# Kernel tuning notes

Hardware: AMD Instinct MI355X
Metric: run time of the kernel (lower is better)

The kernel has to match this reference:

```python
import jax, jax.numpy as jnp
import numpy as np

B, S, E = 2, 2048, 1024
H, D = 16, 64  # NUM_ATTENTION_HEADS, NUM_FEATURES
LN_EPS = 1e-5


def setup_inputs() -> dict:
    key = jax.random.key(0)
    ks = jax.random.split(key, 10)
    scale = 1.0 / np.sqrt(E)
    return {
        "x": jax.random.normal(ks[0], (B, S, E), dtype=jnp.float32),
        "ln_g": jnp.ones((E,), dtype=jnp.float32),
        "ln_b": jnp.zeros((E,), dtype=jnp.float32),
        "wq": jax.random.normal(ks[1], (E, H * D), dtype=jnp.float32) * scale,
        "bq": jnp.zeros((H * D,), dtype=jnp.float32),
        "wk": jax.random.normal(ks[2], (E, H * D), dtype=jnp.float32) * scale,
        "bk": jnp.zeros((H * D,), dtype=jnp.float32),
        "wv": jax.random.normal(ks[3], (E, H * D), dtype=jnp.float32) * scale,
        "bv": jnp.zeros((H * D,), dtype=jnp.float32),
        "wo": jax.random.normal(ks[4], (H * D, E), dtype=jnp.float32) * scale,
        "bo": jnp.zeros((E,), dtype=jnp.float32),
    }


def reference(x, ln_g, ln_b, wq, bq, wk, bk, wv, bv, wo, bo):
    x_residual = x
    # LayerNorm over last dim
    mean = jnp.mean(x, axis=-1, keepdims=True)
    var = jnp.mean(jnp.square(x - mean), axis=-1, keepdims=True)
    xn = (x - mean) * jax.lax.rsqrt(var + LN_EPS) * ln_g + ln_b

    q = (xn @ wq + bq).reshape(B, S, H, D)
    k = (xn @ wk + bk).reshape(B, S, H, D)
    v = (xn @ wv + bv).reshape(B, S, H, D)

    # scores: [B, S_q, S_k, H]
    score = jnp.einsum('bihd,bjhd->bijh', q, k) / np.sqrt(D).astype(np.float32)
    # causal mask: position i may not attend to j > i
    causal = jnp.tril(jnp.ones((S, S), dtype=bool))  # True = keep
    score = jnp.where(causal[None, :, :, None], score, -jnp.inf)
    probs = jax.nn.softmax(score, axis=2)

    out = jnp.einsum('bijh,bjhd->bihd', probs, v).reshape(B, S, H * D)
    out = out @ wo + bo
    return out + x_residual
```

## Files before the change

kernel.cpp:

```cpp
#include <hip/hip_runtime.h>
#include <math.h>
#include <stdint.h>

typedef short short8 __attribute__((ext_vector_type(8)));
typedef short s16x4 __attribute__((ext_vector_type(4)));
typedef float f32x4 __attribute__((ext_vector_type(4)));

constexpr int BB = 2, SS = 2048, EE = 1024, HH = 16, DD = 64, HD = 1024;
constexpr int NROW = BB * SS;
constexpr size_t WELEM = (size_t)1024 * 1024;
constexpr float LN_EPS = 1e-5f;

__device__ const int ENT_QT[40] = {0,1,2,3, 4,4, 5,5, 6,6, 7,7,
                                   8,8,8, 9,9,9, 10,10,10, 11,11,11,
                                   12,12,12,12, 13,13,13,13, 14,14,14,14, 15,15,15,15};
__device__ const int ENT_C0[40] = {0,0,0,0, 0,1, 0,1, 0,1, 0,1,
                                   0,1,2, 0,1,2, 0,1,2, 0,1,2,
                                   0,1,2,3, 0,1,2,3, 0,1,2,3, 0,1,2,3};
__device__ const int EBASE[16]  = {0,1,2,3,4,6,8,10,12,15,18,21,24,28,32,36};
constexpr int NENT = 40;

#if defined(__has_builtin)
#if __has_builtin(__builtin_amdgcn_exp2f)
#define EXP2F(x) __builtin_amdgcn_exp2f(x)
#endif
#endif
#ifndef EXP2F
#define EXP2F(x) exp2f(x)
#endif

__device__ inline short f2bf(float f) {
    union { float f; uint32_t u; } v; v.f = f;
    uint32_t r = (v.u + 0x7fffu + ((v.u >> 16) & 1u)) >> 16;
    return (short)(uint16_t)r;
}

__device__ inline float bf2f(short s) {
    return __uint_as_float(((uint32_t)(uint16_t)s) << 16);
}

__device__ inline uint32_t pk2bf(float f0, float f1) {
    uint32_t u0 = __float_as_uint(f0) + 0x8000u;
    uint32_t u1 = __float_as_uint(f1) + 0x8000u;
    return __builtin_amdgcn_perm(u1, u0, 0x07060302u);
}

__device__ inline uint32_t pk2bf_t(float f0, float f1) {
    return __builtin_amdgcn_perm(__float_as_uint(f1), __float_as_uint(f0), 0x07060302u);
}

__device__ inline s16x4 pack_bf16x4(f32x4 v) {
    union { uint32_t u[2]; s16x4 s; } r;
    r.u[0] = pk2bf(v[0], v[1]);
    r.u[1] = pk2bf(v[2], v[3]);
    return r.s;
}

#define GLOBAL_TO_LDS16(g, l) \
    __builtin_amdgcn_global_load_lds( \
        (const __attribute__((address_space(1))) void*)(g), \
        (__attribute__((address_space(3))) void*)(l), 16, 0, 0)

__global__ void prep_kernel(const float* __restrict__ x,
                            const float* __restrict__ g,
                            const float* __restrict__ b,
                            short* __restrict__ xn,
                            const float* __restrict__ w0, const float* __restrict__ w1,
                            const float* __restrict__ w2, const float* __restrict__ w3,
                            short* __restrict__ wdst) {
    const int bx = blockIdx.x;
    const int t = threadIdx.x;
    if (bx < NROW) {
        const int row = bx;
        const float* xr = x + (size_t)row * EE;
        short* onr = xn + (size_t)row * EE;
        float4 v = ((const float4*)xr)[t];
        float s  = v.x + v.y + v.z + v.w;
        float ss = v.x * v.x + v.y * v.y + v.z * v.z + v.w * v.w;
        #pragma unroll
        for (int o = 32; o > 0; o >>= 1) {
            s  += __shfl_down(s, o);
            ss += __shfl_down(ss, o);
        }
        __shared__ float sm[4], sm2[4];
        const int wid = t >> 6, lane = t & 63;
        if (lane == 0) { sm[wid] = s; sm2[wid] = ss; }
        __syncthreads();
        float ts  = sm[0] + sm[1] + sm[2] + sm[3];
        float tss = sm2[0] + sm2[1] + sm2[2] + sm2[3];
        float mean = ts * (1.0f / EE);
        float var  = tss * (1.0f / EE) - mean * mean;
        float inv  = rsqrtf(var + LN_EPS);
        float4 gv = ((const float4*)g)[t];
        float4 bv = ((const float4*)b)[t];
        s16x4 st;
        st.x = f2bf((v.x - mean) * inv * gv.x + bv.x);
        st.y = f2bf((v.y - mean) * inv * gv.y + bv.y);
        st.z = f2bf((v.z - mean) * inv * gv.z + bv.z);
        st.w = f2bf((v.w - mean) * inv * gv.w + bv.w);
        ((s16x4*)onr)[t] = st;
    } else {
        const int widx = bx - NROW;
        const int z = widx >> 10;
        const int rem = widx & 1023;
        const int k0 = (rem >> 5) * 32, p0 = (rem & 31) * 32;
        const float* src = (z == 0) ? w0 : (z == 1) ? w1 : (z == 2) ? w2 : w3;
        short* d = wdst + (size_t)z * WELEM;
        __shared__ float tile[32][33];
        const int tx = t & 31, ty = t >> 5;
        #pragma unroll
        for (int r = ty; r < 32; r += 8)
            tile[r][tx] = src[(size_t)(k0 + r) * 1024 + p0 + tx];
        __syncthreads();
        #pragma unroll
        for (int r = ty; r < 32; r += 8)
            d[(size_t)(p0 + r) * 1024 + k0 + tx] = f2bf(tile[tx][r]);
    }
}

template <bool F32OUT>
__global__ __launch_bounds__(256) void mfma_gemm(
    const short* __restrict__ A,
    const short* __restrict__ BtBase,
    const float* __restrict__ b0, const float* __restrict__ b1,
    const float* __restrict__ b2,
    short* __restrict__ outB, short* __restrict__ outV,
    const float* __restrict__ resid, float* __restrict__ outF) {
    constexpr int K = 1024, N = 1024;
    const int t = threadIdx.x, lane = t & 63, w = t >> 6;
    const int quad = lane >> 4, l16 = lane & 15;
    const int wm = w >> 1, wn = w & 1;
    const int row0 = blockIdx.y * 128, col0 = blockIdx.x * 128;
    const int z = blockIdx.z;
    const short* Bt = BtBase + (size_t)z * WELEM;
    const float* bias = (z == 0) ? b0 : (z == 1) ? b1 : b2;

    __shared__ short As[128 * 32];
    __shared__ short Bs[128 * 32];

    f32x4 acc[4][4];
    #pragma unroll
    for (int i = 0; i < 4; i++)
        #pragma unroll
        for (int j = 0; j < 4; j++) acc[i][j] = (f32x4){0.f, 0.f, 0.f, 0.f};

    const int srow = t >> 2, schunk = t & 3;
    const short* agp = A  + (size_t)(row0 + srow) * K + schunk * 8;
    const short* bgp = Bt + (size_t)(col0 + srow) * K + schunk * 8;

    for (int k0 = 0; k0 < K; k0 += 32) {
        GLOBAL_TO_LDS16(agp + k0,                    As + t * 8);
        GLOBAL_TO_LDS16(agp + (size_t)64 * K + k0,   As + 2048 + t * 8);
        GLOBAL_TO_LDS16(bgp + k0,                    Bs + t * 8);
        GLOBAL_TO_LDS16(bgp + (size_t)64 * K + k0,   Bs + 2048 + t * 8);
        __syncthreads();
        short8 af[4], bf[4];
        #pragma unroll
        for (int mt = 0; mt < 4; mt++)
            af[mt] = *(const short8*)&As[(wm * 64 + mt * 16 + l16) * 32 + quad * 8];
        #pragma unroll
        for (int nt = 0; nt < 4; nt++)
            bf[nt] = *(const short8*)&Bs[(wn * 64 + nt * 16 + l16) * 32 + quad * 8];
        #pragma unroll
        for (int mt = 0; mt < 4; mt++)
            #pragma unroll
            for (int nt = 0; nt < 4; nt++)
                acc[mt][nt] = __builtin_amdgcn_mfma_f32_16x16x32_bf16(
                    af[mt], bf[nt], acc[mt][nt], 0, 0, 0);
        __syncthreads();
    }

    #pragma unroll
    for (int mt = 0; mt < 4; mt++) {
        #pragma unroll
        for (int nt = 0; nt < 4; nt++) {
            const int rbase = row0 + wm * 64 + mt * 16 + quad * 4;
            const int col = col0 + wn * 64 + nt * 16 + l16;
            const float bcol = bias[col];
            if (F32OUT) {
                #pragma unroll
                for (int r = 0; r < 4; r++)
                    outF[(size_t)(rbase + r) * N + col] =
                        acc[mt][nt][r] + bcol +
                        resid[(size_t)(rbase + r) * N + col];
            } else if (z == 2) {
                union { uint32_t u[2]; s16x4 s; } pk;
                pk.u[0] = pk2bf(acc[mt][nt][0] + bcol, acc[mt][nt][1] + bcol);
                pk.u[1] = pk2bf(acc[mt][nt][2] + bcol, acc[mt][nt][3] + bcol);
                *(s16x4*)&outV[(size_t)col * NROW + rbase] = pk.s;
            } else {
                #pragma unroll
                for (int r = 0; r < 4; r++)
                    outB[(size_t)z * NROW * N + (size_t)(rbase + r) * N + col] =
                        f2bf(acc[mt][nt][r] + bcol);
            }
        }
    }
}

#define ATTN_ITER(JT, DIAG)                                                     \
    {                                                                           \
        const int jt_ = (JT);                                                   \
        if (jt_ + 1 < jt1) {                                                    \
            const size_t ko = (size_t)(jt_ + 1) * 64 * HD;                      \
            const int vo = (jt_ + 1) * 64;                                      \
            const int ob = (buf ^ 1) * 4096;                                    \
            GLOBAL_TO_LDS16(kb0 + ko, Kb + ob + t * 8);                         \
            GLOBAL_TO_LDS16(kb1 + ko, Kb + ob + (t + 256) * 8);                 \
            GLOBAL_TO_LDS16(vb0 + vo, Vb + ob + t * 8);                         \
            GLOBAL_TO_LDS16(vb1 + vo, Vb + ob + (t + 256) * 8);                 \
        }                                                                       \
        const short* Kc = Kb + buf * 4096;                                      \
        const short* Vc = Vb + buf * 4096;                                      \
        f32x4 s[4][2];                                                          \
        _Pragma("unroll")                                                       \
        for (int mj = 0; mj < 4; mj++)                                          \
            _Pragma("unroll")                                                   \
            for (int nt = 0; nt < 2; nt++) s[mj][nt] = (f32x4){0.f,0.f,0.f,0.f};\
        _Pragma("unroll")                                                       \
        for (int ks = 0; ks < 2; ks++) {                                        \
            const int cq = ((ks * 4 + quad) ^ sw) * 8;                          \
            short8 kf[4], qf[2];                                                \
            _Pragma("unroll")                                                   \
            for (int mj = 0; mj < 4; mj++)                                      \
                kf[mj] = *(const short8*)&Kc[(mj * 16 + l16) * 64 + cq];        \
            _Pragma("unroll")                                                   \
            for (int nt = 0; nt < 2; nt++)                                      \
                qf[nt] = *(const short8*)&Qs[(w * 32 + nt * 16 + l16) * 64 + cq];\
            _Pragma("unroll")                                                   \
            for (int mj = 0; mj < 4; mj++)                                      \
                _Pragma("unroll")                                               \
                for (int nt = 0; nt < 2; nt++)                                  \
                    s[mj][nt] = __builtin_amdgcn_mfma_f32_16x16x32_bf16(        \
                        kf[mj], qf[nt], s[mj][nt], 0, 0, 0);                    \
        }                                                                       \
        const int joff = (jt_ - 2 * qt) * 64;                                   \
        _Pragma("unroll")                                                       \
        for (int mj = 0; mj < 4; mj++) {                                        \
            _Pragma("unroll")                                                   \
            for (int nt = 0; nt < 2; nt++) {                                    \
                const int ir = irel + nt * 16;                                  \
                _Pragma("unroll")                                               \
                for (int r = 0; r < 4; r++) {                                   \
                    float p = EXP2F(s[mj][nt][r] * 0.18033688f);                \
                    if (DIAG) {                                                 \
                        const int jrel = joff + mj * 16 + quad * 4 + r;         \
                        if (jrel > ir) p = 0.f;                                 \
                    }                                                           \
                    s[mj][nt][r] = p;                                           \
                }                                                               \
            }                                                                   \
        }                                                                       \
        _Pragma("unroll")                                                       \
        for (int ks2 = 0; ks2 < 4; ks2++) {                                     \
            s16x4 pf[2];                                                        \
            _Pragma("unroll")                                                   \
            for (int nt = 0; nt < 2; nt++) {                                    \
                union { uint32_t u[2]; s16x4 s4; } r_;                          \
                r_.u[0] = pk2bf_t(s[ks2][nt][0], s[ks2][nt][1]);                \
                r_.u[1] = pk2bf_t(s[ks2][nt][2], s[ks2][nt][3]);                \
                pf[nt] = r_.s4;                                                 \
                Lacc[nt] = __builtin_amdgcn_mfma_f32_16x16x16bf16_1k(           \
                    onesf, pf[nt], Lacc[nt], 0, 0, 0);                          \
            }                                                                   \
            _Pragma("unroll")                                                   \
            for (int mtd = 0; mtd < 4; mtd++) {                                 \
                const int cv = (((ks2 * 2 + (quad >> 1)) ^ sw) * 8) + (quad & 1) * 4;\
                s16x4 vf = *(const s16x4*)&Vc[(mtd * 16 + l16) * 64 + cv];      \
                _Pragma("unroll")                                               \
                for (int nt = 0; nt < 2; nt++)                                  \
                    Ot[mtd][nt] = __builtin_amdgcn_mfma_f32_16x16x16bf16_1k(    \
                        vf, pf[nt], Ot[mtd][nt], 0, 0, 0);                      \
            }                                                                   \
        }                                                                       \
        __syncthreads();                                                        \
        buf ^= 1;                                                               \
    }

__global__ __launch_bounds__(256) void attn_split(
    const short* __restrict__ q, const short* __restrict__ kkk,
    const short* __restrict__ vtp,
    short* __restrict__ OpartB, float* __restrict__ lpart,
    short* __restrict__ attno) {
    const int e = NENT - 1 - (int)blockIdx.x;
    const int h = blockIdx.y, b = blockIdx.z;
    const int qt = ENT_QT[e], c0 = ENT_C0[e];
    const int t = threadIdx.x, lane = t & 63, w = t >> 6;
    const int quad = lane >> 4, l16 = lane & 15;
    const int sw = l16 & 7;
    const int i0 = qt * 128;

    __shared__ short Qs[128 * 64];
    __shared__ short Kb[2 * 64 * 64];
    __shared__ short Vb[2 * 64 * 64];

    const size_t qoff = ((size_t)(b * SS + i0)) * HD + h * DD;
    #pragma unroll
    for (int p = 0; p < 4; p++) {
        const int idx = t + p * 256;
        const int r = idx >> 3, cs = idx & 7;
        const int c = cs ^ (r & 7);
        GLOBAL_TO_LDS16(q + qoff + (size_t)r * HD + c * 8, Qs + idx * 8);
    }

    const int r0 = t >> 3,         cs0 = t & 7;
    const int r1 = (t + 256) >> 3, cs1 = (t + 256) & 7;
    const short* kb0 = kkk + ((size_t)b * SS) * HD + h * DD + (size_t)r0 * HD + (cs0 ^ (r0 & 7)) * 8;
    const short* kb1 = kkk + ((size_t)b * SS) * HD + h * DD + (size_t)r1 * HD + (cs1 ^ (r1 & 7)) * 8;
    const short* vb0 = vtp + ((size_t)(h * 64 + r0)) * NROW + b * SS + (cs0 ^ (r0 & 7)) * 8;
    const short* vb1 = vtp + ((size_t)(h * 64 + r1)) * NROW + b * SS + (cs1 ^ (r1 & 7)) * 8;

    f32x4 Ot[4][2];
    f32x4 Lacc[2];
    #pragma unroll
    for (int mtd = 0; mtd < 4; mtd++)
        #pragma unroll
        for (int nt = 0; nt < 2; nt++) Ot[mtd][nt] = (f32x4){0.f, 0.f, 0.f, 0.f};
    Lacc[0] = (f32x4){0.f, 0.f, 0.f, 0.f};
    Lacc[1] = (f32x4){0.f, 0.f, 0.f, 0.f};
    s16x4 onesf;
    onesf[0] = onesf[1] = onesf[2] = onesf[3] = (short)0x3F80;

    const int jt0 = c0 * 8;
    const int jt1 = min(jt0 + 8, 2 * qt + 2);
    const int irel = w * 32 + l16;

    {
        const size_t ko = (size_t)jt0 * 64 * HD;
        const int vo = jt0 * 64;
        GLOBAL_TO_LDS16(kb0 + ko, Kb + t * 8);
        GLOBAL_TO_LDS16(kb1 + ko, Kb + (t + 256) * 8);
        GLOBAL_TO_LDS16(vb0 + vo, Vb + t * 8);
        GLOBAL_TO_LDS16(vb1 + vo, Vb + (t + 256) * 8);
    }
    __syncthreads();

    int buf = 0;
    const int dmid   = min(jt1, 2 * qt);
    const int dstart = max(jt0, 2 * qt);
    for (int jt = jt0; jt < dmid; ++jt) ATTN_ITER(jt, false)
    for (int jt = dstart; jt < jt1; ++jt) ATTN_ITER(jt, true)

    if (qt < 4) {
        #pragma unroll
        for (int nt = 0; nt < 2; nt++) {
            const float inv = 1.0f / Lacc[nt][0];
            const int i_abs = i0 + w * 32 + nt * 16 + l16;
            const size_t ob = ((size_t)(b * SS + i_abs)) * HD + h * DD;
            #pragma unroll
            for (int mtd = 0; mtd < 4; mtd++) {
                f32x4 val = Ot[mtd][nt];
                union { uint32_t u[2]; s16x4 s4; } pk;
                pk.u[0] = pk2bf(val[0] * inv, val[1] * inv);
                pk.u[1] = pk2bf(val[2] * inv, val[3] * inv);
                *(s16x4*)&attno[ob + mtd * 16 + quad * 4] = pk.s4;
            }
        }
    } else {
        const int slot = (b * HH + h) * NENT + e;
        #pragma unroll
        for (int nt = 0; nt < 2; nt++) {
            const int i_rel = w * 32 + nt * 16 + l16;
            if (quad == 0) lpart[(size_t)slot * 128 + i_rel] = Lacc[nt][0];
            #pragma unroll
            for (int mtd = 0; mtd < 4; mtd++)
                *(s16x4*)&OpartB[(size_t)slot * 8192 + i_rel * 64 + mtd * 16 + quad * 4] =
                    pack_bf16x4(Ot[mtd][nt]);
        }
    }
}

__global__ __launch_bounds__(256) void attn_reduce(
    const short* __restrict__ OpartB, const float* __restrict__ lpart,
    short* __restrict__ attno) {
    const int qt = 4 + blockIdx.x, h = blockIdx.y, b = blockIdx.z;
    const int t = threadIdx.x;
    const int nch = (qt >> 2) + 1;
    const int slot0 = (b * HH + h) * NENT + EBASE[qt];
    const int i0 = qt * 128;
    #pragma unroll
    for (int it = 0; it < 8; it++) {
        const int g = t + it * 256;
        const int i = g >> 4, d4 = (g & 15) * 4;
        f32x4 acc = (f32x4){0.f, 0.f, 0.f, 0.f};
        float l = 0.f;
        for (int c = 0; c < nch; c++) {
            s16x4 pv = *(const s16x4*)&OpartB[(size_t)(slot0 + c) * 8192 + i * 64 + d4];
            acc[0] += bf2f(pv[0]);
            acc[1] += bf2f(pv[1]);
            acc[2] += bf2f(pv[2]);
            acc[3] += bf2f(pv[3]);
            l += lpart[(size_t)(slot0 + c) * 128 + i];
        }
        const float inv = 1.0f / l;
        union { uint32_t u[2]; s16x4 s; } pk;
        pk.u[0] = pk2bf(acc[0] * inv, acc[1] * inv);
        pk.u[1] = pk2bf(acc[2] * inv, acc[3] * inv);
        *(s16x4*)&attno[((size_t)(b * SS + i0 + i)) * HD + h * DD + d4] = pk.s;
    }
}

extern "C" void kernel_launch(void* const* d_in, const int* in_sizes, int n_in,
                              void* d_out, int out_size, void* d_ws, size_t ws_size,
                              hipStream_t stream) {
    const float* x    = (const float*)d_in[0];
    const float* ln_g = (const float*)d_in[1];
    const float* ln_b = (const float*)d_in[2];
    const float* wq   = (const float*)d_in[3];
    const float* bq   = (const float*)d_in[4];
    const float* wk   = (const float*)d_in[5];
    const float* bk   = (const float*)d_in[6];
    const float* wv   = (const float*)d_in[7];
    const float* bv   = (const float*)d_in[8];
    const float* wo   = (const float*)d_in[9];
    const float* bo   = (const float*)d_in[10];
    float* out = (float*)d_out;

    const size_t buf = (size_t)NROW * HD;
    short* xn    = (short*)d_ws;
    short* qb    = xn + buf;
    short* vt    = qb + 2 * buf;
    short* attno = vt + buf;
    short* wt    = attno + buf;
    short* OpB   = wt + 4 * WELEM;
    float* lpart = (float*)(OpB + (size_t)BB * HH * NENT * 8192);

    prep_kernel<<<2 * NROW, 256, 0, stream>>>(x, ln_g, ln_b, xn, wq, wk, wv, wo, wt);

    mfma_gemm<false><<<dim3(8, 32, 3), 256, 0, stream>>>(
        xn, wt, bq, bk, bv, qb, vt, nullptr, nullptr);

    attn_split<<<dim3(NENT, HH, BB), 256, 0, stream>>>(
        qb, qb + buf, vt, OpB, lpart, attno);
    attn_reduce<<<dim3(12, HH, BB), 256, 0, stream>>>(OpB, lpart, attno);

    mfma_gemm<true><<<dim3(8, 32, 1), 256, 0, stream>>>(
        attno, wt + 3 * WELEM, bo, bo, bo, nullptr, nullptr, x, out);
}
```

Before: 207.6 us.

## Fuse split-K attention reduction into attn_split via atomic counters; keep Q in registers

Removes the separate attn_reduce launch. Each split block writes its partial results, then bumps a per-(b,h,qt) atomic counter, and the last-arriving block performs the reduction and normalisation. The counters are zeroed in prep_kernel. Q fragments are now loaded straight into registers instead of being staged through LDS, and launch bounds request 4 blocks per SM. This saves a kernel launch and LDS traffic, at the cost of threadfence/atomic overhead and higher register pressure.

```diff
diff --git a/kernel.cpp b/kernel.cpp
--- a/kernel.cpp
+++ b/kernel.cpp
@@ -67,10 +67,14 @@
                             short* __restrict__ xn,
                             const float* __restrict__ w0, const float* __restrict__ w1,
                             const float* __restrict__ w2, const float* __restrict__ w3,
-                            short* __restrict__ wdst) {
+                            short* __restrict__ wdst, int* __restrict__ cnt) {
     const int bx = blockIdx.x;
     const int t = threadIdx.x;
     if (bx < NROW) {
+        if (bx == 0) {
+            cnt[t] = 0;
+            if (t < 128) cnt[256 + t] = 0;
+        }
         const int row = bx;
         const float* xr = x + (size_t)row * EE;
         short* onr = xn + (size_t)row * EE;
@@ -220,19 +224,16 @@
         _Pragma("unroll")                                                       \
         for (int ks = 0; ks < 2; ks++) {                                        \
             const int cq = ((ks * 4 + quad) ^ sw) * 8;                          \
-            short8 kf[4], qf[2];                                                \
+            short8 kf[4];                                                       \
             _Pragma("unroll")                                                   \
             for (int mj = 0; mj < 4; mj++)                                      \
                 kf[mj] = *(const short8*)&Kc[(mj * 16 + l16) * 64 + cq];        \
-            _Pragma("unroll")                                                   \
-            for (int nt = 0; nt < 2; nt++)                                      \
-                qf[nt] = *(const short8*)&Qs[(w * 32 + nt * 16 + l16) * 64 + cq];\
             _Pragma("unroll")                                                   \
             for (int mj = 0; mj < 4; mj++)                                      \
                 _Pragma("unroll")                                               \
                 for (int nt = 0; nt < 2; nt++)                                  \
                     s[mj][nt] = __builtin_amdgcn_mfma_f32_16x16x32_bf16(        \
-                        kf[mj], qf[nt], s[mj][nt], 0, 0, 0);                    \
+                        kf[mj], qreg[nt][ks], s[mj][nt], 0, 0, 0);              \
         }                                                                       \
         const int joff = (jt_ - 2 * qt) * 64;                                   \
         _Pragma("unroll")                                                       \
@@ -277,11 +278,11 @@
         buf ^= 1;                                                               \
     }
 
-__global__ __launch_bounds__(256) void attn_split(
+__global__ __launch_bounds__(256, 4) void attn_split(
     const short* __restrict__ q, const short* __restrict__ kkk,
     const short* __restrict__ vtp,
     short* __restrict__ OpartB, float* __restrict__ lpart,
-    short* __restrict__ attno) {
+    short* __restrict__ attno, int* __restrict__ cnt) {
     const int e = NENT - 1 - (int)blockIdx.x;
     const int h = blockIdx.y, b = blockIdx.z;
     const int qt = ENT_QT[e], c0 = ENT_C0[e];
@@ -290,18 +291,18 @@
     const int sw = l16 & 7;
     const int i0 = qt * 128;
 
-    __shared__ short Qs[128 * 64];
     __shared__ short Kb[2 * 64 * 64];
     __shared__ short Vb[2 * 64 * 64];
-
+    __shared__ int oldc_s;
+
+    short8 qreg[2][2];
     const size_t qoff = ((size_t)(b * SS + i0)) * HD + h * DD;
+    const short* qrow = q + qoff + (size_t)(w * 32 + l16) * HD + quad * 8;
     #pragma unroll
-    for (int p = 0; p < 4; p++) {
-        const int idx = t + p * 256;
-        const int r = idx >> 3, cs = idx & 7;
-        const int c = cs ^ (r & 7);
-        GLOBAL_TO_LDS16(q + qoff + (size_t)r * HD + c * 8, Qs + idx * 8);
-    }
+    for (int nt = 0; nt < 2; nt++)
+        #pragma unroll
+        for (int ks = 0; ks < 2; ks++)
+            qreg[nt][ks] = *(const short8*)(qrow + nt * 16 * HD + ks * 32);
 
     const int r0 = t >> 3,         cs0 = t & 7;
     const int r1 = (t + 256) >> 3, cs1 = (t + 256) & 7;
@@ -356,47 +357,50 @@
                 *(s16x4*)&attno[ob + mtd * 16 + quad * 4] = pk.s4;
             }
         }
-    } else {
-        const int slot = (b * HH + h) * NENT + e;
-        #pragma unroll
-        for (int nt = 0; nt < 2; nt++) {
-            const int i_rel = w * 32 + nt * 16 + l16;
-            if (quad == 0) lpart[(size_t)slot * 128 + i_rel] = Lacc[nt][0];
-            #pragma unroll
-            for (int mtd = 0; mtd < 4; mtd++)
-                *(s16x4*)&OpartB[(size_t)slot * 8192 + i_rel * 64 + mtd * 16 + quad * 4] =
-                    pack_bf16x4(Ot[mtd][nt]);
+        return;
+    }
+
+    const int slot = (b * HH + h) * NENT + e;
+    #pragma unroll
+    for (int nt = 0; nt < 2; nt++) {
+        const int i_rel = w * 32 + nt * 16 + l16;
+        if (quad == 0) lpart[(size_t)slot * 128 + i_rel] = Lacc[nt][0];
+        #pragma unroll
+        for (int mtd = 0; mtd < 4; mtd++)
+            *(s16x4*)&OpartB[(size_t)slot * 8192 + i_rel * 64 + mtd * 16 + quad * 4] =
+                pack_bf16x4(Ot[mtd][nt]);
+    }
+    __syncthreads();
+
+    const int nch = (qt >> 2) + 1;
+    if (t == 0) {
+        __threadfence();
+        oldc_s = atomicAdd(&cnt[(b * HH + h) * 12 + (qt - 4)], 1);
+    }
+    __syncthreads();
+    if (oldc_s == nch - 1) {
+        __threadfence();
+        const int slot0 = (b * HH + h) * NENT + EBASE[qt];
+        #pragma unroll
+        for (int it = 0; it < 8; it++) {
+            const int gg = t + it * 256;
+            const int i = gg >> 4, d4 = (gg & 15) * 4;
+            f32x4 acc = (f32x4){0.f, 0.f, 0.f, 0.f};
+            float l = 0.f;
+            for (int c = 0; c < nch; c++) {
+                s16x4 pv = *(const s16x4*)&OpartB[(size_t)(slot0 + c) * 8192 + i * 64 + d4];
+                acc[0] += bf2f(pv[0]);
+                acc[1] += bf2f(pv[1]);
+                acc[2] += bf2f(pv[2]);
+                acc[3] += bf2f(pv[3]);
+                l += lpart[(size_t)(slot0 + c) * 128 + i];
+            }
+            const float inv = 1.0f / l;
+            union { uint32_t u[2]; s16x4 s4; } pk;
+            pk.u[0] = pk2bf(acc[0] * inv, acc[1] * inv);
+            pk.u[1] = pk2bf(acc[2] * inv, acc[3] * inv);
+            *(s16x4*)&attno[((size_t)(b * SS + i0 + i)) * HD + h * DD + d4] = pk.s4;
         }
-    }
-}
-
-__global__ __launch_bounds__(256) void attn_reduce(
-    const short* __restrict__ OpartB, const float* __restrict__ lpart,
-    short* __restrict__ attno) {
-    const int qt = 4 + blockIdx.x, h = blockIdx.y, b = blockIdx.z;
-    const int t = threadIdx.x;
-    const int nch = (qt >> 2) + 1;
-    const int slot0 = (b * HH + h) * NENT + EBASE[qt];
-    const int i0 = qt * 128;
-    #pragma unroll
-    for (int it = 0; it < 8; it++) {
-        const int g = t + it * 256;
-        const int i = g >> 4, d4 = (g & 15) * 4;
-        f32x4 acc = (f32x4){0.f, 0.f, 0.f, 0.f};
-        float l = 0.f;
-        for (int c = 0; c < nch; c++) {
-            s16x4 pv = *(const s16x4*)&OpartB[(size_t)(slot0 + c) * 8192 + i * 64 + d4];
-            acc[0] += bf2f(pv[0]);
-            acc[1] += bf2f(pv[1]);
-            acc[2] += bf2f(pv[2]);
-            acc[3] += bf2f(pv[3]);
-            l += lpart[(size_t)(slot0 + c) * 128 + i];
-        }
-        const float inv = 1.0f / l;
-        union { uint32_t u[2]; s16x4 s; } pk;
-        pk.u[0] = pk2bf(acc[0] * inv, acc[1] * inv);
-        pk.u[1] = pk2bf(acc[2] * inv, acc[3] * inv);
-        *(s16x4*)&attno[((size_t)(b * SS + i0 + i)) * HD + h * DD + d4] = pk.s;
     }
 }
 
@@ -424,15 +428,16 @@
     short* wt    = attno + buf;
     short* OpB   = wt + 4 * WELEM;
     float* lpart = (float*)(OpB + (size_t)BB * HH * NENT * 8192);
-
-    prep_kernel<<<2 * NROW, 256, 0, stream>>>(x, ln_g, ln_b, xn, wq, wk, wv, wo, wt);
+    int*   cnt   = (int*)(lpart + (size_t)BB * HH * NENT * 128);
+
+    prep_kernel<<<2 * NROW, 256, 0, stream>>>(x, ln_g, ln_b, xn,
+                                              wq, wk, wv, wo, wt, cnt);
 
     mfma_gemm<false><<<dim3(8, 32, 3), 256, 0, stream>>>(
         xn, wt, bq, bk, bv, qb, vt, nullptr, nullptr);
 
     attn_split<<<dim3(NENT, HH, BB), 256, 0, stream>>>(
-        qb, qb + buf, vt, OpB, lpart, attno);
-    attn_reduce<<<dim3(12, HH, BB), 256, 0, stream>>>(OpB, lpart, attno);
+        qb, qb + buf, vt, OpB, lpart, attno, cnt);
 
     mfma_gemm<true><<<dim3(8, 32, 1), 256, 0, stream>>>(
         attno, wt + 3 * WELEM, bo, bo, bo, nullptr, nullptr, x, out);
```

New measurement: 372.2 us. +79.3%, slower.
